# Optimization experiments

Hardware: AMD Instinct MI355X
Metric: run time of the kernel (lower is better)

The kernel has to match this reference:

```python
import jax, jax.numpy as jnp
import numpy as np

SCORE_THRESHOLD = 0.5
IOU_THRESHOLD = 0.5
N = 8192
IMG = 640.0


def setup_inputs() -> dict:
    key = jax.random.key(0)
    k1, k2, k3 = jax.random.split(key, 3)
    # valid xyxy boxes on a 640px canvas: x2 > x1, y2 > y1
    xy1 = jax.random.uniform(k1, (N, 2), dtype=jnp.float32) * (IMG - 64.0)
    wh = jax.random.uniform(k2, (N, 2), dtype=jnp.float32) * 96.0 + 4.0
    xyxy = jnp.concatenate([xy1, xy1 + wh], axis=1)  # [N,4]
    person_conf = jax.random.uniform(k3, (N,), dtype=jnp.float32)  # [N]
    return {"xyxy": xyxy, "person_conf": person_conf}


def _pairwise_iou(boxes):
    # boxes: [N,4] xyxy -> iou: [N,N]
    x1, y1, x2, y2 = boxes[:, 0], boxes[:, 1], boxes[:, 2], boxes[:, 3]
    area = (x2 - x1) * (y2 - y1)  # [N]
    ix1 = jnp.maximum(x1[:, None], x1[None, :])
    iy1 = jnp.maximum(y1[:, None], y1[None, :])
    ix2 = jnp.minimum(x2[:, None], x2[None, :])
    iy2 = jnp.minimum(y2[:, None], y2[None, :])
    iw = jnp.maximum(ix2 - ix1, 0.0)
    ih = jnp.maximum(iy2 - iy1, 0.0)
    inter = iw * ih
    union = area[:, None] + area[None, :] - inter
    return inter / jnp.maximum(union, 1e-9)


def reference(xyxy, person_conf):
    # score-threshold filter (as a mask to stay jit-compatible / fixed shape)
    valid = person_conf >= SCORE_THRESHOLD  # [N]
    # sort by score descending; invalid boxes sink to the bottom
    sort_scores = jnp.where(valid, person_conf, -jnp.inf)
    order = jnp.argsort(-sort_scores)  # [N]
    boxes_s = xyxy[order]              # [N,4]
    scores_s = person_conf[order]      # [N]
    valid_s = valid[order]             # [N]

    iou = _pairwise_iou(boxes_s)  # [N,N]
    idx = jnp.arange(N)

    def body(i, keep):
        # box i (if still kept) suppresses lower-scored overlapping boxes
        sup = keep[i] & (iou[i] > IOU_THRESHOLD) & (idx > i)
        return keep & ~sup

    keep = jax.lax.fori_loop(0, N, body, valid_s)  # [N] bool

    boxes_and_scores = jnp.concatenate([boxes_s, scores_s[:, None]], axis=1)  # [N,5]
    out = jnp.where(keep[:, None], boxes_and_scores, 0.0)  # suppressed rows zeroed
    return out, keep
```

## Files before the change

### kernel.cpp

```cpp
#include <hip/hip_runtime.h>

typedef unsigned long long u64;
typedef unsigned int u32;

static constexpr int N = 8192;
static constexpr int NW = N / 64;
static constexpr int CAPE = 12288;
static constexpr int EPT = CAPE / 1024;


__device__ __forceinline__ u64 make_key(float s, int i) {
  u32 adj = (s >= 0.5f) ? (__float_as_uint(s) + 1u) : 0u;
  return ((u64)adj << 32) | (u64)(u32)(N - 1 - i);
}

__global__ __launch_bounds__(1024)
void rank_scatter_kernel(const float4* __restrict__ xyxy, const float* __restrict__ conf,
                         float4* __restrict__ boxes_s, float* __restrict__ scores_s,
                         float* __restrict__ areas_s,
                         int* __restrict__ ecount, int* __restrict__ done) {
  #pragma clang fp contract(off)
  __shared__ u64 sk[2048];
  __shared__ u32 cnt[64];
  const int tid = threadIdx.x;
  const int il = tid & 63;
  const int jq = tid >> 6;
  const int i = blockIdx.x * 64 + il;
  if (tid < 64) cnt[tid] = 0;
  if (blockIdx.x == 0 && tid == 0) { *ecount = 0; *done = 0; }
  const u64 ki = make_key(conf[i], i);
  u32 local = 0;
  for (int tile = 0; tile < 4; ++tile) {
    __syncthreads();
    int j0 = tile * 2048 + tid;
    sk[tid] = make_key(conf[j0], j0);
    int j1 = j0 + 1024;
    sk[1024 + tid] = make_key(conf[j1], j1);
    __syncthreads();
    const int base = jq * 128;
    #pragma unroll 8
    for (int k = 0; k < 128; ++k) local += (sk[base + k] > ki);
  }
  atomicAdd(&cnt[il], local);
  __syncthreads();
  if (tid < 64) {
    u32 r = cnt[tid];
    int ii = blockIdx.x * 64 + tid;
    float4 b = xyxy[ii];
    boxes_s[r] = b;
    scores_s[r] = conf[ii];
    areas_s[r] = (b.z - b.x) * (b.w - b.y);
  }
}

__global__ __launch_bounds__(1024)
void mask_reduce_kernel(const float4* __restrict__ boxes_s,
                        const float* __restrict__ areas_s,
                        const float* __restrict__ scores_s,
                        u64* __restrict__ edgeW, u32* __restrict__ edgeM,
                        int* __restrict__ ecount, int* __restrict__ done,
                        float* __restrict__ out) {
  #pragma clang fp contract(off)
  __shared__ float4 cb[16][64];
  __shared__ float  ca[16][64];
  __shared__ u32 keep32[2 * NW];
  __shared__ u32 valid32[2 * NW];
  __shared__ u32 ext32[2 * NW];
  __shared__ u32 loc32[2][64];
  __shared__ int chg[2];
  __shared__ int lastsh;
  const int tid = threadIdx.x;
  const int lane = tid & 63;
  const int wave = tid >> 6;
  const int yb = blockIdx.y;

  #pragma unroll
  for (int q = 0; q < 2; ++q) {
    const int xb = blockIdx.x * 32 + wave * 2 + q;
    if (xb < yb || scores_s[xb * 64] < 0.5f) continue;
    cb[wave][lane] = boxes_s[xb * 64 + lane];
    ca[wave][lane] = areas_s[xb * 64 + lane];
    const int i = yb * 64 + lane;
    const float4 rb = boxes_s[i];
    const float ra = areas_s[i];
    const float sc_i = scores_s[i];
    const int jbase = xb * 64;
    u64 w = 0;
    for (int p = 0; p < 64; ++p) {
      float4 c = cb[wave][p];
      float ix1 = fmaxf(rb.x, c.x);
      float iy1 = fmaxf(rb.y, c.y);
      float ix2 = fminf(rb.z, c.z);
      float iy2 = fminf(rb.w, c.w);
      float iw = fmaxf(ix2 - ix1, 0.0f);
      float ih = fmaxf(iy2 - iy1, 0.0f);
      float inter = iw * ih;
      float uni = fmaxf((ra + ca[wave][p]) - inter, 1e-9f);
      float iou = inter / uni;
      if ((iou > 0.5f) && (jbase + p > i)) w |= (1ull << p);
    }
    if (sc_i < 0.5f) w = 0;
    u64 nz = __ballot(w != 0ull);
    if (nz) {
      int base = 0;
      if (lane == 0) base = atomicAdd(ecount, __popcll(nz));
      base = __shfl(base, 0);
      if (w) {
        int idx = base + __popcll(nz & ((1ull << lane) - 1ull));
        if (idx < CAPE) {
          __hip_atomic_store(&edgeW[idx], w,
                             __ATOMIC_RELAXED, __HIP_MEMORY_SCOPE_AGENT);
          __hip_atomic_store(&edgeM[idx], (u32)i | ((u32)xb << 16),
                             __ATOMIC_RELAXED, __HIP_MEMORY_SCOPE_AGENT);
        }
      }
    }
  }

  __syncthreads();
  if (tid == 0)
    lastsh = (atomicAdd(done, 1) == (int)(gridDim.x * gridDim.y) - 1);
  __syncthreads();
  if (!lastsh) return;

  for (int p = tid; p < N; p += 1024) {
    u64 b = __ballot(scores_s[p] >= 0.5f);
    if (lane == 0) {
      valid32[(p >> 6) * 2]     = (u32)b;
      valid32[(p >> 6) * 2 + 1] = (u32)(b >> 32);
    }
  }
  if (tid < 256) ext32[tid] = 0;
  if (tid < 64)  loc32[0][tid] = 0;
  if (tid >= 64 && tid < 128) loc32[1][tid - 64] = 0;

  int E = __hip_atomic_load(ecount, __ATOMIC_RELAXED, __HIP_MEMORY_SCOPE_AGENT);
  if (E > CAPE) E = CAPE;
  u64 ew[EPT]; u32 em[EPT]; int ne = 0;
  #pragma unroll
  for (int k = 0; k < EPT; ++k) {
    int e = tid + k * 1024;
    if (e < E) {
      ew[k] = __hip_atomic_load(&edgeW[e], __ATOMIC_RELAXED, __HIP_MEMORY_SCOPE_AGENT);
      em[k] = __hip_atomic_load(&edgeM[e], __ATOMIC_RELAXED, __HIP_MEMORY_SCOPE_AGENT);
      ne = k + 1;
    } else { ew[k] = 0; em[k] = 0; }
  }
  __syncthreads();

  for (int s = 0; s < 4; ++s) {
    if (tid < 64) {
      int wI = s * 64 + tid;
      keep32[wI] = valid32[wI] & ~ext32[wI];
    }
    if (tid == 0) { chg[0] = 0; chg[1] = 0; }
    __syncthreads();
    int par = 0;
    for (int it = 0; it < 4096; ++it) {
      #pragma unroll
      for (int k = 0; k < EPT; ++k) {
        if (k < ne) {
          int row = em[k] & 0xffff;
          int x = em[k] >> 16;
          if ((row >> 11) == s && (x >> 5) == s) {
            if ((keep32[row >> 5] >> (row & 31)) & 1u) {
              atomicOr(&loc32[par][2 * (x & 31)],     (u32)ew[k]);
              atomicOr(&loc32[par][2 * (x & 31) + 1], (u32)(ew[k] >> 32));
            }
          }
        }
      }
      __syncthreads();
      if (tid < 64) {
        int wI = s * 64 + tid;
        u32 nk = valid32[wI] & ~ext32[wI] & ~loc32[par][tid];
        if (nk != keep32[wI]) { keep32[wI] = nk; chg[par] = 1; }
        loc32[par ^ 1][tid] = 0;
      }
      if (tid == 64) chg[par ^ 1] = 0;
      __syncthreads();
      if (!chg[par]) break;
      par ^= 1;
    }
    #pragma unroll
    for (int k = 0; k < EPT; ++k) {
      if (k < ne) {
        int row = em[k] & 0xffff;
        int x = em[k] >> 16;
        if ((row >> 11) == s && (x >> 5) != s) {
          if ((keep32[row >> 5] >> (row & 31)) & 1u) {
            atomicOr(&ext32[2 * x],     (u32)ew[k]);
            atomicOr(&ext32[2 * x + 1], (u32)(ew[k] >> 32));
          }
        }
      }
    }
    if (tid < 64)  loc32[0][tid] = 0;
    if (tid >= 64 && tid < 128) loc32[1][tid - 64] = 0;
    __syncthreads();
  }

  for (int s = tid; s < N; s += 1024) {
    bool keep = (keep32[s >> 5] >> (s & 31)) & 1u;
    float4 b = boxes_s[s];
    float sc = scores_s[s];
    float* row = out + (u64)s * 5;
    if (keep) {
      row[0] = b.x; row[1] = b.y; row[2] = b.z; row[3] = b.w; row[4] = sc;
      out[N * 5 + s] = 1.0f;
    } else {
      row[0] = 0.0f; row[1] = 0.0f; row[2] = 0.0f; row[3] = 0.0f; row[4] = 0.0f;
      out[N * 5 + s] = 0.0f;
    }
  }
}

extern "C" void kernel_launch(void* const* d_in, const int* in_sizes, int n_in,
                              void* d_out, int out_size, void* d_ws, size_t ws_size,
                              hipStream_t stream) {
  const float4* xyxy = (const float4*)d_in[0];
  const float* conf  = (const float*)d_in[1];
  char* ws = (char*)d_ws;
  float4* boxes_s   = (float4*)(ws + 0);
  float*  scores_s  = (float*)(ws + 131072);
  float*  areas_s   = (float*)(ws + 163840);
  int*    ecount    = (int*)(ws + 196608);
  int*    done      = (int*)(ws + 196612);
  u64*    edgeW     = (u64*)(ws + 196672);
  u32*    edgeM     = (u32*)(ws + 294976);
  float*  out       = (float*)d_out;

  rank_scatter_kernel<<<N / 64, 1024, 0, stream>>>(xyxy, conf, boxes_s,
                                                   scores_s, areas_s,
                                                   ecount, done);
  dim3 mg(4, NW);
  mask_reduce_kernel<<<mg, 1024, 0, stream>>>(boxes_s, areas_s, scores_s,
                                              edgeW, edgeM, ecount, done, out);
}
```

Measured before the change: 118.6 us.

## Split mask/fix/write into separate kernels and bucket edges in LDS

The last-block-done tail is replaced by separate kernels: the mask computation, a single-block 256-thread fix kernel, and a parallel write kernel across many blocks. The fix kernel copies edges into LDS, bucketed by diagonal-versus-cross segment, so each pass scans only the edges that matter. Before, every one of 1024 threads tested every register-held edge against the segment filter. The IoU division is replaced by a double-precision multiply comparison. This adds two kernel launches and uses large LDS arrays (about 144KB) in the fix kernel.

```diff
diff --git a/kernel.cpp b/kernel.cpp
--- a/kernel.cpp
+++ b/kernel.cpp
@@ -6,7 +6,6 @@
 static constexpr int N = 8192;
 static constexpr int NW = N / 64;
 static constexpr int CAPE = 12288;
-static constexpr int EPT = CAPE / 1024;
 
 
 __device__ __forceinline__ u64 make_key(float s, int i) {
@@ -17,8 +16,7 @@
 __global__ __launch_bounds__(1024)
 void rank_scatter_kernel(const float4* __restrict__ xyxy, const float* __restrict__ conf,
                          float4* __restrict__ boxes_s, float* __restrict__ scores_s,
-                         float* __restrict__ areas_s,
-                         int* __restrict__ ecount, int* __restrict__ done) {
+                         float* __restrict__ areas_s, int* __restrict__ ecount) {
   #pragma clang fp contract(off)
   __shared__ u64 sk[2048];
   __shared__ u32 cnt[64];
@@ -27,7 +25,7 @@
   const int jq = tid >> 6;
   const int i = blockIdx.x * 64 + il;
   if (tid < 64) cnt[tid] = 0;
-  if (blockIdx.x == 0 && tid == 0) { *ecount = 0; *done = 0; }
+  if (blockIdx.x == 0 && tid == 0) *ecount = 0;
   const u64 ki = make_key(conf[i], i);
   u32 local = 0;
   for (int tile = 0; tile < 4; ++tile) {
@@ -54,26 +52,18 @@
 }
 
 __global__ __launch_bounds__(1024)
-void mask_reduce_kernel(const float4* __restrict__ boxes_s,
-                        const float* __restrict__ areas_s,
-                        const float* __restrict__ scores_s,
-                        u64* __restrict__ edgeW, u32* __restrict__ edgeM,
-                        int* __restrict__ ecount, int* __restrict__ done,
-                        float* __restrict__ out) {
+void mask_kernel(const float4* __restrict__ boxes_s, const float* __restrict__ areas_s,
+                 const float* __restrict__ scores_s,
+                 u64* __restrict__ edgeW, u32* __restrict__ edgeM,
+                 int* __restrict__ ecount) {
   #pragma clang fp contract(off)
   __shared__ float4 cb[16][64];
   __shared__ float  ca[16][64];
-  __shared__ u32 keep32[2 * NW];
-  __shared__ u32 valid32[2 * NW];
-  __shared__ u32 ext32[2 * NW];
-  __shared__ u32 loc32[2][64];
-  __shared__ int chg[2];
-  __shared__ int lastsh;
   const int tid = threadIdx.x;
   const int lane = tid & 63;
   const int wave = tid >> 6;
   const int yb = blockIdx.y;
-
+  const double C = 0.5 + 0x1p-25;
   #pragma unroll
   for (int q = 0; q < 2; ++q) {
     const int xb = blockIdx.x * 32 + wave * 2 + q;
@@ -96,8 +86,8 @@
       float ih = fmaxf(iy2 - iy1, 0.0f);
       float inter = iw * ih;
       float uni = fmaxf((ra + ca[wave][p]) - inter, 1e-9f);
-      float iou = inter / uni;
-      if ((iou > 0.5f) && (jbase + p > i)) w |= (1ull << p);
+      bool sup = ((double)inter > C * (double)uni);
+      if (sup && (jbase + p > i)) w |= (1ull << p);
     }
     if (sc_i < 0.5f) w = 0;
     u64 nz = __ballot(w != 0ull);
@@ -108,73 +98,89 @@
       if (w) {
         int idx = base + __popcll(nz & ((1ull << lane) - 1ull));
         if (idx < CAPE) {
-          __hip_atomic_store(&edgeW[idx], w,
-                             __ATOMIC_RELAXED, __HIP_MEMORY_SCOPE_AGENT);
-          __hip_atomic_store(&edgeM[idx], (u32)i | ((u32)xb << 16),
-                             __ATOMIC_RELAXED, __HIP_MEMORY_SCOPE_AGENT);
+          edgeW[idx] = w;
+          edgeM[idx] = (u32)i | ((u32)xb << 16);
         }
       }
     }
   }
-
-  __syncthreads();
-  if (tid == 0)
-    lastsh = (atomicAdd(done, 1) == (int)(gridDim.x * gridDim.y) - 1);
-  __syncthreads();
-  if (!lastsh) return;
-
-  for (int p = tid; p < N; p += 1024) {
+}
+
+__global__ __launch_bounds__(256)
+void fix_kernel(const u64* __restrict__ edgeWG, const u32* __restrict__ edgeMG,
+                const int* __restrict__ ecount, const float* __restrict__ scores_s,
+                u64* __restrict__ keepw) {
+  __shared__ u64 ew[CAPE];
+  __shared__ u32 em[CAPE];
+  __shared__ u32 valid32[2 * NW];
+  __shared__ u32 ext32[2 * NW];
+  __shared__ u32 keep32[2 * NW];
+  __shared__ u32 loc32[2][64];
+  __shared__ u32 bcnt[8], boff[8];
+  __shared__ int chg[2];
+  const int tid = threadIdx.x;
+  const int lane = tid & 63;
+
+  if (tid < 8) bcnt[tid] = 0;
+  if (tid < 256) ext32[tid] = 0;
+  if (tid < 128) loc32[tid >> 6][tid & 63] = 0;
+  for (int p = tid; p < N; p += 256) {
     u64 b = __ballot(scores_s[p] >= 0.5f);
     if (lane == 0) {
       valid32[(p >> 6) * 2]     = (u32)b;
       valid32[(p >> 6) * 2 + 1] = (u32)(b >> 32);
     }
   }
-  if (tid < 256) ext32[tid] = 0;
-  if (tid < 64)  loc32[0][tid] = 0;
-  if (tid >= 64 && tid < 128) loc32[1][tid - 64] = 0;
-
-  int E = __hip_atomic_load(ecount, __ATOMIC_RELAXED, __HIP_MEMORY_SCOPE_AGENT);
+  int E = *ecount;
   if (E > CAPE) E = CAPE;
-  u64 ew[EPT]; u32 em[EPT]; int ne = 0;
-  #pragma unroll
-  for (int k = 0; k < EPT; ++k) {
-    int e = tid + k * 1024;
-    if (e < E) {
-      ew[k] = __hip_atomic_load(&edgeW[e], __ATOMIC_RELAXED, __HIP_MEMORY_SCOPE_AGENT);
-      em[k] = __hip_atomic_load(&edgeM[e], __ATOMIC_RELAXED, __HIP_MEMORY_SCOPE_AGENT);
-      ne = k + 1;
-    } else { ew[k] = 0; em[k] = 0; }
+  __syncthreads();
+
+  for (int e = tid; e < E; e += 256) {
+    u32 m = edgeMG[e];
+    int s = (m & 0xffff) >> 11, xs = (m >> 16) >> 5;
+    atomicAdd(&bcnt[s * 2 + (xs != s)], 1u);
+  }
+  __syncthreads();
+  if (tid == 0) {
+    u32 acc = 0;
+    #pragma unroll
+    for (int b = 0; b < 8; ++b) { boff[b] = acc; acc += bcnt[b]; bcnt[b] = boff[b]; }
+  }
+  __syncthreads();
+  for (int e = tid; e < E; e += 256) {
+    u32 m = edgeMG[e];
+    int s = (m & 0xffff) >> 11, xs = (m >> 16) >> 5;
+    u32 idx = atomicAdd(&bcnt[s * 2 + (xs != s)], 1u);
+    ew[idx] = edgeWG[e];
+    em[idx] = m;
   }
   __syncthreads();
 
   for (int s = 0; s < 4; ++s) {
     if (tid < 64) {
-      int wI = s * 64 + tid;
-      keep32[wI] = valid32[wI] & ~ext32[wI];
+      keep32[s * 64 + tid] = valid32[s * 64 + tid] & ~ext32[s * 64 + tid];
     }
     if (tid == 0) { chg[0] = 0; chg[1] = 0; }
     __syncthreads();
+    const u32 l0 = boff[s * 2], l1 = boff[s * 2] + (bcnt[s * 2] - boff[s * 2]);
+    const u32 lend = bcnt[s * 2];
+    (void)l1;
     int par = 0;
     for (int it = 0; it < 4096; ++it) {
-      #pragma unroll
-      for (int k = 0; k < EPT; ++k) {
-        if (k < ne) {
-          int row = em[k] & 0xffff;
-          int x = em[k] >> 16;
-          if ((row >> 11) == s && (x >> 5) == s) {
-            if ((keep32[row >> 5] >> (row & 31)) & 1u) {
-              atomicOr(&loc32[par][2 * (x & 31)],     (u32)ew[k]);
-              atomicOr(&loc32[par][2 * (x & 31) + 1], (u32)(ew[k] >> 32));
-            }
-          }
+      for (u32 e = l0 + tid; e < lend; e += 256) {
+        u32 m = em[e];
+        int row = m & 0xffff;
+        if ((keep32[row >> 5] >> (row & 31)) & 1u) {
+          int x = m >> 16;
+          u64 w = ew[e];
+          atomicOr(&loc32[par][2 * (x & 31)],     (u32)w);
+          atomicOr(&loc32[par][2 * (x & 31) + 1], (u32)(w >> 32));
         }
       }
       __syncthreads();
       if (tid < 64) {
-        int wI = s * 64 + tid;
-        u32 nk = valid32[wI] & ~ext32[wI] & ~loc32[par][tid];
-        if (nk != keep32[wI]) { keep32[wI] = nk; chg[par] = 1; }
+        u32 nk = valid32[s * 64 + tid] & ~ext32[s * 64 + tid] & ~loc32[par][tid];
+        if (nk != keep32[s * 64 + tid]) { keep32[s * 64 + tid] = nk; chg[par] = 1; }
         loc32[par ^ 1][tid] = 0;
       }
       if (tid == 64) chg[par ^ 1] = 0;
@@ -182,36 +188,38 @@
       if (!chg[par]) break;
       par ^= 1;
     }
-    #pragma unroll
-    for (int k = 0; k < EPT; ++k) {
-      if (k < ne) {
-        int row = em[k] & 0xffff;
-        int x = em[k] >> 16;
-        if ((row >> 11) == s && (x >> 5) != s) {
-          if ((keep32[row >> 5] >> (row & 31)) & 1u) {
-            atomicOr(&ext32[2 * x],     (u32)ew[k]);
-            atomicOr(&ext32[2 * x + 1], (u32)(ew[k] >> 32));
-          }
-        }
-      }
-    }
-    if (tid < 64)  loc32[0][tid] = 0;
-    if (tid >= 64 && tid < 128) loc32[1][tid - 64] = 0;
-    __syncthreads();
-  }
-
-  for (int s = tid; s < N; s += 1024) {
-    bool keep = (keep32[s >> 5] >> (s & 31)) & 1u;
-    float4 b = boxes_s[s];
-    float sc = scores_s[s];
-    float* row = out + (u64)s * 5;
-    if (keep) {
-      row[0] = b.x; row[1] = b.y; row[2] = b.z; row[3] = b.w; row[4] = sc;
-      out[N * 5 + s] = 1.0f;
-    } else {
-      row[0] = 0.0f; row[1] = 0.0f; row[2] = 0.0f; row[3] = 0.0f; row[4] = 0.0f;
-      out[N * 5 + s] = 0.0f;
-    }
+    const u32 x0 = boff[s * 2 + 1], xend = bcnt[s * 2 + 1];
+    for (u32 e = x0 + tid; e < xend; e += 256) {
+      u32 m = em[e];
+      int row = m & 0xffff;
+      if ((keep32[row >> 5] >> (row & 31)) & 1u) {
+        int x = m >> 16;
+        u64 w = ew[e];
+        atomicOr(&ext32[2 * x],     (u32)w);
+        atomicOr(&ext32[2 * x + 1], (u32)(w >> 32));
+      }
+    }
+    if (tid < 128) loc32[tid >> 6][tid & 63] = 0;
+    __syncthreads();
+  }
+  if (tid < 128)
+    keepw[tid] = ((u64)keep32[2 * tid + 1] << 32) | (u64)keep32[2 * tid];
+}
+
+__global__ __launch_bounds__(256)
+void write_kernel(const float4* __restrict__ boxes_s, const float* __restrict__ scores_s,
+                  const u64* __restrict__ keepw, float* __restrict__ out) {
+  const int s = blockIdx.x * 256 + threadIdx.x;
+  bool keep = (keepw[s >> 6] >> (s & 63)) & 1ull;
+  float4 b = boxes_s[s];
+  float sc = scores_s[s];
+  float* row = out + (u64)s * 5;
+  if (keep) {
+    row[0] = b.x; row[1] = b.y; row[2] = b.z; row[3] = b.w; row[4] = sc;
+    out[N * 5 + s] = 1.0f;
+  } else {
+    row[0] = 0.0f; row[1] = 0.0f; row[2] = 0.0f; row[3] = 0.0f; row[4] = 0.0f;
+    out[N * 5 + s] = 0.0f;
   }
 }
 
@@ -225,15 +233,16 @@
   float*  scores_s  = (float*)(ws + 131072);
   float*  areas_s   = (float*)(ws + 163840);
   int*    ecount    = (int*)(ws + 196608);
-  int*    done      = (int*)(ws + 196612);
-  u64*    edgeW     = (u64*)(ws + 196672);
-  u32*    edgeM     = (u32*)(ws + 294976);
+  u64*    keepw     = (u64*)(ws + 196616);
+  u64*    edgeW     = (u64*)(ws + 197696);
+  u32*    edgeM     = (u32*)(ws + 296000);
   float*  out       = (float*)d_out;
 
   rank_scatter_kernel<<<N / 64, 1024, 0, stream>>>(xyxy, conf, boxes_s,
-                                                   scores_s, areas_s,
-                                                   ecount, done);
+                                                   scores_s, areas_s, ecount);
   dim3 mg(4, NW);
-  mask_reduce_kernel<<<mg, 1024, 0, stream>>>(boxes_s, areas_s, scores_s,
-                                              edgeW, edgeM, ecount, done, out);
-}
+  mask_kernel<<<mg, 1024, 0, stream>>>(boxes_s, areas_s, scores_s,
+                                       edgeW, edgeM, ecount);
+  fix_kernel<<<1, 256, 0, stream>>>(edgeW, edgeM, ecount, scores_s, keepw);
+  write_kernel<<<N / 256, 256, 0, stream>>>(boxes_s, scores_s, keepw, out);
+}
```

Result: slower. 129.2 us (+9.0%).
